# Kernel tuning notes

Measured on AMD Instinct MI355X. Metric: run time of the kernel, lower is better.

The kernel has to match this reference:

```python
import jax, jax.numpy as jnp
import numpy as np

T = 16          # timesteps
BATCH = 8       # video clips -> leading dim of x is BATCH*T = 128
C_IN = 768      # fixed by nn.Conv2d(768, redu_dim, 1)
D = 256         # redu_dim
K = 64          # num_centers
H = W = 28
EPS = 1e-12     # torch F.normalize eps


def _conv(x, w, padding):
    # x: [N,C,H,W], w: [O,I,kh,kw]
    return jax.lax.conv_general_dilated(
        x, w, window_strides=(1, 1), padding=padding,
        dimension_numbers=('NCHW', 'OIHW', 'NCHW'))


def setup_inputs() -> dict:
    key = jax.random.key(0)
    ks = jax.random.split(key, 9)
    x = jax.random.normal(ks[0], (BATCH * T, C_IN, H, W), dtype=jnp.float32)
    redu_w = jax.random.normal(ks[1], (D, C_IN, 1, 1), jnp.float32) * 0.02
    redu_b = jnp.zeros((D,), jnp.float32)
    share_w = jax.random.normal(ks[2], (K, D, 1, 1), jnp.float32) * 0.05
    share_b = jnp.zeros((K,), jnp.float32)
    U_z = jax.random.normal(ks[3], (K, K, 3, 3), jnp.float32) * 0.04
    U_r = jax.random.normal(ks[4], (K, K, 3, 3), jnp.float32) * 0.04
    U_h = jax.random.normal(ks[5], (K, K, 3, 3), jnp.float32) * 0.04
    centers = jax.random.normal(ks[6], (K, D), jnp.float32) * 0.06
    return {"x": x, "redu_w": redu_w, "redu_b": redu_b,
            "share_w": share_w, "share_b": share_b,
            "U_z": U_z, "U_r": U_r, "U_h": U_h,
            "centers": centers, "timesteps": T}


def reference(x, redu_w, redu_b, share_w, share_b, U_z, U_r, U_h, centers, timesteps):
    t = timesteps
    bt, _, h, w = x.shape
    b = bt // t
    k = share_w.shape[0]
    d = redu_w.shape[0]

    # channel reduction (1x1 conv)
    xr = _conv(x, redu_w, 'VALID') + redu_b[None, :, None, None]        # [bt,d,h,w]
    # shared assignment logits (1x1 conv)
    wxb = _conv(xr, share_w, 'VALID') + share_b[None, :, None, None]     # [bt,k,h,w]
    wxb = wxb.reshape(b, t, k, h, w).transpose(1, 0, 2, 3, 4)            # [t,b,k,h,w]

    # sequential ConvGRU over timesteps
    h0 = jnp.zeros((b, k, h, w), x.dtype)
    def step(h_tm1, w_t):
        z = jax.nn.sigmoid(w_t + _conv(h_tm1, U_z, 'SAME'))
        r = jax.nn.sigmoid(w_t + _conv(h_tm1, U_r, 'SAME'))
        hh = jnp.tanh(w_t + _conv(r * h_tm1, U_h, 'SAME'))
        h_new = (1.0 - z) * hh + z * h_tm1
        return h_new, h_new
    _, hs = jax.lax.scan(step, h0, wxb)                                  # [t,b,k,h,w]

    assign = hs.transpose(1, 0, 2, 3, 4).reshape(b * t, k, h * w)        # [bt,k,hw]
    # softmax over centers per spatial location
    assign = jax.nn.softmax(assign, axis=1)

    # VLAD aggregation
    a_sum = assign.sum(axis=-1, keepdims=True)                           # [bt,k,1]
    a = a_sum * centers[None]                                            # [bt,k,d]
    xf = xr.reshape(b * t, d, h * w)                                     # [bt,d,hw]
    vlad = jnp.einsum('bkp,bdp->bkd', assign, xf) - a                    # [bt,k,d]

    vlad = vlad.reshape(b, t, k, d).sum(axis=1)                          # [b,k,d]
    # intra-norm over feature dim, then global L2 norm
    vlad = vlad / jnp.maximum(jnp.linalg.norm(vlad, axis=2, keepdims=True), EPS)
    vlad = vlad.reshape(b, k * d)
    vlad = vlad / jnp.maximum(jnp.linalg.norm(vlad, axis=1, keepdims=True), EPS)
    return vlad
```

## Files before the change

### kernel.cpp

```cpp
#include <hip/hip_runtime.h>
#include <hip/hip_bf16.h>

#define T_ 16
#define B_ 8
#define CIN 768
#define D_ 256
#define K_ 64
#define HW 784
#define W_ 28

typedef short short8 __attribute__((ext_vector_type(8)));
typedef short short4v __attribute__((ext_vector_type(4)));
typedef float floatx4 __attribute__((ext_vector_type(4)));
typedef unsigned short ushort_t;

__device__ __forceinline__ unsigned short f2bf(float x) {
    union { float f; unsigned u; } v; v.f = x;
    unsigned u = v.u;
    unsigned r = (u + 0x7fffu + ((u >> 16) & 1u)) >> 16;
    return (unsigned short)r;
}
__device__ __forceinline__ float bf2f(unsigned short h) {
    union { unsigned u; float f; } v; v.u = ((unsigned)h) << 16; return v.f;
}

__device__ __forceinline__ float block_reduce_sum_256(float v) {
    for (int off = 32; off > 0; off >>= 1) v += __shfl_down(v, off, 64);
    __shared__ float red[4];
    __shared__ float tot;
    int lane = threadIdx.x & 63, wid = threadIdx.x >> 6;
    if (lane == 0) red[wid] = v;
    __syncthreads();
    if (threadIdx.x == 0) tot = red[0] + red[1] + red[2] + red[3];
    __syncthreads();
    return tot;
}

__global__ __launch_bounds__(256) void cvt_weights(
    const float* __restrict__ rw, const float* __restrict__ sw,
    const float* __restrict__ Uz, const float* __restrict__ Ur,
    const float* __restrict__ Uh,
    ushort_t* __restrict__ whi, ushort_t* __restrict__ wlo,
    ushort_t* __restrict__ shi, ushort_t* __restrict__ slo,
    ushort_t* __restrict__ azh, ushort_t* __restrict__ azl,
    ushort_t* __restrict__ ahh, ushort_t* __restrict__ ahl)
{
    int i = blockIdx.x * 256 + threadIdx.x;
    const int nR = D_ * CIN;
    const int nS = K_ * D_;
    const int nZR = 128 * 576;
    const int nH = 64 * 576;
    if (i < nR) {
        float x = rw[i];
        unsigned short h = f2bf(x);
        whi[i] = h; wlo[i] = f2bf(x - bf2f(h));
    } else if (i < nR + nS) {
        int j = i - nR;
        float x = sw[j];
        unsigned short h = f2bf(x);
        shi[j] = h; slo[j] = f2bf(x - bf2f(h));
    } else if (i < nR + nS + nZR) {
        int j = i - nR - nS;
        int row = j / 576, kk = j - row * 576;
        int tap = kk >> 6, c = kk & 63;
        const float* U = (row < 64) ? Uz : Ur;
        float x = U[(((size_t)(row & 63)) * 64 + c) * 9 + tap];
        unsigned short h = f2bf(x);
        azh[j] = h; azl[j] = f2bf(x - bf2f(h));
    } else if (i < nR + nS + nZR + nH) {
        int j = i - nR - nS - nZR;
        int row = j / 576, kk = j - row * 576;
        int tap = kk >> 6, c = kk & 63;
        float x = Uh[(((size_t)row) * 64 + c) * 9 + tap];
        unsigned short h = f2bf(x);
        ahh[j] = h; ahl[j] = f2bf(x - bf2f(h));
    }
}

template<int BM, int KD>
__global__ __launch_bounds__(256, 2) void mfma_conv1x1(
    const float* __restrict__ X, const ushort_t* __restrict__ Whi,
    const ushort_t* __restrict__ Wlo, const float* __restrict__ bias,
    float* __restrict__ Out)
{
    const int nt = blockIdx.x, bt = blockIdx.z;
    const int p0 = nt * 112;
    const int tid = threadIdx.x, lane = tid & 63, wv = tid >> 6;
    const float* Xb = X + (size_t)bt * KD * HW;
    float* Ob = Out + (size_t)bt * BM * HW;

    __shared__ ushort_t lB[2][112 * 40];

    constexpr int NI = (BM == 256) ? 7 : 2;
    constexpr int NKS = KD / 32;
    floatx4 acc[4][NI];
#pragma unroll
    for (int a = 0; a < 4; ++a)
#pragma unroll
        for (int b = 0; b < NI; ++b) acc[a][b] = (floatx4){0.f, 0.f, 0.f, 0.f};

    const int koff = (lane >> 4) * 8;
    const int li = lane & 15;
    const int mbase = (BM == 256) ? wv * 64 : 0;

    const int u0j = tid / 112, u0p = tid - u0j * 112;
    const bool u1v = tid < 192;
    const int u1j = (tid + 256) / 112, u1p = (tid + 256) - u1j * 112;

    float b0[16], b1[16];
    short8 ahi[4], alo[4];

    auto loadB = [&](int k0, float* bb) {
        const float* xp0 = Xb + (size_t)(k0 + u0j * 8) * HW + p0 + u0p;
#pragma unroll
        for (int c = 0; c < 8; ++c) bb[c] = xp0[c * HW];
        if (u1v) {
            const float* xp1 = Xb + (size_t)(k0 + u1j * 8) * HW + p0 + u1p;
#pragma unroll
            for (int c = 0; c < 8; ++c) bb[8 + c] = xp1[c * HW];
        }
    };
    auto writeB = [&](const float* bb) {
        short8 vh, vl;
#pragma unroll
        for (int c = 0; c < 8; ++c) {
            unsigned short h = f2bf(bb[c]);
            vh[c] = (short)h; vl[c] = (short)f2bf(bb[c] - bf2f(h));
        }
        *(short8*)&lB[0][u0p * 40 + u0j * 8] = vh;
        *(short8*)&lB[1][u0p * 40 + u0j * 8] = vl;
        if (u1v) {
#pragma unroll
            for (int c = 0; c < 8; ++c) {
                unsigned short h = f2bf(bb[8 + c]);
                vh[c] = (short)h; vl[c] = (short)f2bf(bb[8 + c] - bf2f(h));
            }
            *(short8*)&lB[0][u1p * 40 + u1j * 8] = vh;
            *(short8*)&lB[1][u1p * 40 + u1j * 8] = vl;
        }
    };
    auto loadA = [&](int k0) {
#pragma unroll
        for (int mi = 0; mi < 4; ++mi) {
            int m = mbase + mi * 16 + li;
            ahi[mi] = *(const short8*)(Whi + (size_t)m * KD + k0 + koff);
            alo[mi] = *(const short8*)(Wlo + (size_t)m * KD + k0 + koff);
        }
    };
    auto domfma = [&]() {
        if constexpr (BM == 256) {
#pragma unroll
            for (int ni = 0; ni < 7; ++ni) {
                int n = ni * 16 + li;
                short8 bhi = *(const short8*)&lB[0][n * 40 + koff];
                short8 blo = *(const short8*)&lB[1][n * 40 + koff];
#pragma unroll
                for (int mi = 0; mi < 4; ++mi) {
                    acc[mi][ni] = __builtin_amdgcn_mfma_f32_16x16x32_bf16(ahi[mi], bhi, acc[mi][ni], 0, 0, 0);
                    acc[mi][ni] = __builtin_amdgcn_mfma_f32_16x16x32_bf16(ahi[mi], blo, acc[mi][ni], 0, 0, 0);
                    acc[mi][ni] = __builtin_amdgcn_mfma_f32_16x16x32_bf16(alo[mi], bhi, acc[mi][ni], 0, 0, 0);
                }
            }
        } else {
#pragma unroll
            for (int nj = 0; nj < 2; ++nj) {
                int ni = wv * 2 + nj;
                if (ni >= 7) break;
                int n = ni * 16 + li;
                short8 bhi = *(const short8*)&lB[0][n * 40 + koff];
                short8 blo = *(const short8*)&lB[1][n * 40 + koff];
#pragma unroll
                for (int mi = 0; mi < 4; ++mi) {
                    acc[mi][nj] = __builtin_amdgcn_mfma_f32_16x16x32_bf16(ahi[mi], bhi, acc[mi][nj], 0, 0, 0);
                    acc[mi][nj] = __builtin_amdgcn_mfma_f32_16x16x32_bf16(ahi[mi], blo, acc[mi][nj], 0, 0, 0);
                    acc[mi][nj] = __builtin_amdgcn_mfma_f32_16x16x32_bf16(alo[mi], bhi, acc[mi][nj], 0, 0, 0);
                }
            }
        }
    };

    loadB(0, b0);
    for (int ks = 0; ks < NKS; ks += 2) {
        loadA(ks * 32);
        writeB(b0);
        __syncthreads();
        if (ks + 1 < NKS) loadB((ks + 1) * 32, b1);
        domfma();
        __syncthreads();
        loadA((ks + 1) * 32);
        writeB(b1);
        __syncthreads();
        if (ks + 2 < NKS) loadB((ks + 2) * 32, b0);
        domfma();
        __syncthreads();
    }

    if constexpr (BM == 256) {
#pragma unroll
        for (int mi = 0; mi < 4; ++mi) {
            int m0g = wv * 64 + mi * 16 + ((lane >> 4) << 2);
#pragma unroll
            for (int ni = 0; ni < 7; ++ni) {
                int p = p0 + ni * 16 + li;
#pragma unroll
                for (int r = 0; r < 4; ++r)
                    Ob[(size_t)(m0g + r) * HW + p] = acc[mi][ni][r] + bias[m0g + r];
            }
        }
    } else {
#pragma unroll
        for (int nj = 0; nj < 2; ++nj) {
            int ni = wv * 2 + nj;
            if (ni >= 7) break;
            int p = p0 + ni * 16 + li;
#pragma unroll
            for (int mi = 0; mi < 4; ++mi) {
                int m0g = mi * 16 + ((lane >> 4) << 2);
#pragma unroll
                for (int r = 0; r < 4; ++r)
                    Ob[(size_t)(m0g + r) * HW + p] = acc[mi][nj][r] + bias[m0g + r];
            }
        }
    }
}

__global__ __launch_bounds__(512, 2) void gru_step(
    const ushort_t* __restrict__ hRhi, const ushort_t* __restrict__ hRlo,
    ushort_t* __restrict__ hWhi, ushort_t* __restrict__ hWlo,
    const ushort_t* __restrict__ azh, const ushort_t* __restrict__ azl,
    const ushort_t* __restrict__ ahh, const ushort_t* __restrict__ ahl,
    const float* __restrict__ wxb, float* __restrict__ hs_t, int t)
{
    const int y0 = blockIdx.x, b = blockIdx.y;
    const int tid = threadIdx.x, lane = tid & 63, wv = tid >> 6;
    const int li = lane & 15, koff8 = (lane >> 4) * 8, kq = (lane >> 4) * 4;

    __shared__ ushort_t Hhi[5 * 30 * 72], Hlo[5 * 30 * 72];
    __shared__ ushort_t Rhi[3 * 30 * 72], Rlo[3 * 30 * 72];
    __shared__ float zs[28 * 68];

    {
        const ushort_t* gh = hRhi + (size_t)b * HW * 64;
        const ushort_t* gl = hRlo + (size_t)b * HW * 64;
        for (int e = tid; e < 1200; e += 512) {
            int r = e / 240, rem = e - r * 240;
            int lx = rem >> 3, j = rem & 7;
            int gy = y0 - 2 + r, gx = lx - 1;
            short8 vh = {0,0,0,0,0,0,0,0}, vl = {0,0,0,0,0,0,0,0};
            if (gy >= 0 && gy < 28 && gx >= 0 && gx < 28) {
                size_t go = ((size_t)(gy * 28 + gx)) * 64 + j * 8;
                vh = *(const short8*)(gh + go);
                vl = *(const short8*)(gl + go);
            }
            int lo = (r * 30 + lx) * 72 + j * 8;
            *(short8*)&Hhi[lo] = vh;
            *(short8*)&Hlo[lo] = vl;
        }
        short8 z8 = {0,0,0,0,0,0,0,0};
        for (int e = tid; e < 1620; e += 512) {
            if (e < 810) *(short8*)&Rhi[e * 8] = z8;
            else         *(short8*)&Rlo[(e - 810) * 8] = z8;
        }
    }
    __syncthreads();

    const float* wx = wxb + ((size_t)(b * T_ + t) * K_) * HW;
    const int c0 = li;
    const int c1 = (li < 12) ? 16 + li : 0;

    if (wv < 4) {
        const int kb = wv * 16;
        const ushort_t* Ah = azh + (size_t)(kb + li) * 576;
        const ushort_t* Al = azl + (size_t)(kb + li) * 576;
        floatx4 az[2];
        az[0] = (floatx4){0.f,0.f,0.f,0.f}; az[1] = (floatx4){0.f,0.f,0.f,0.f};
#pragma unroll
        for (int tap = 0; tap < 9; ++tap) {
            const int dy = tap / 3, dx = tap - dy * 3;
#pragma unroll
            for (int ch = 0; ch < 2; ++ch) {
                short8 whi_ = *(const short8*)(Ah + tap * 64 + ch * 32 + koff8);
                short8 wlo_ = *(const short8*)(Al + tap * 64 + ch * 32 + koff8);
                int cb = ch * 32 + koff8;
                int o0 = ((dy + 1) * 30 + c0 + dx) * 72 + cb;
                int o1 = ((dy + 1) * 30 + c1 + dx) * 72 + cb;
                short8 bh0 = *(const short8*)&Hhi[o0];
                short8 bl0 = *(const short8*)&Hlo[o0];
                short8 bh1 = *(const short8*)&Hhi[o1];
                short8 bl1 = *(const short8*)&Hlo[o1];
                az[0] = __builtin_amdgcn_mfma_f32_16x16x32_bf16(whi_, bh0, az[0], 0, 0, 0);
                az[0] = __builtin_amdgcn_mfma_f32_16x16x32_bf16(whi_, bl0, az[0], 0, 0, 0);
                az[0] = __builtin_amdgcn_mfma_f32_16x16x32_bf16(wlo_, bh0, az[0], 0, 0, 0);
                az[1] = __builtin_amdgcn_mfma_f32_16x16x32_bf16(whi_, bh1, az[1], 0, 0, 0);
                az[1] = __builtin_amdgcn_mfma_f32_16x16x32_bf16(whi_, bl1, az[1], 0, 0, 0);
                az[1] = __builtin_amdgcn_mfma_f32_16x16x32_bf16(wlo_, bh1, az[1], 0, 0, 0);
            }
        }
        const int kb4 = kb + kq;
#pragma unroll
        for (int cf = 0; cf < 2; ++cf) {
            int c = cf * 16 + li;
            if (c < 28) {
                floatx4 zv;
#pragma unroll
                for (int r = 0; r < 4; ++r)
                    zv[r] = 1.f / (1.f + __expf(-(wx[(size_t)(kb4 + r) * HW + y0 * 28 + c] + az[cf][r])));
                *(floatx4*)&zs[c * 68 + kb4] = zv;
            }
        }
    } else {
        const int kb = (wv - 4) * 16;
        const ushort_t* Ah = azh + (size_t)(64 + kb + li) * 576;
        const ushort_t* Al = azl + (size_t)(64 + kb + li) * 576;
        floatx4 ar[3][2];
#pragma unroll
        for (int i = 0; i < 3; ++i) {
            ar[i][0] = (floatx4){0.f,0.f,0.f,0.f};
            ar[i][1] = (floatx4){0.f,0.f,0.f,0.f};
        }
#pragma unroll
        for (int tap = 0; tap < 9; ++tap) {
            const int dy = tap / 3, dx = tap - dy * 3;
#pragma unroll
            for (int ch = 0; ch < 2; ++ch) {
                short8 whi_ = *(const short8*)(Ah + tap * 64 + ch * 32 + koff8);
                short8 wlo_ = *(const short8*)(Al + tap * 64 + ch * 32 + koff8);
                int cb = ch * 32 + koff8;
#pragma unroll
                for (int rr = 0; rr < 3; ++rr) {
                    int o0 = ((rr + dy) * 30 + c0 + dx) * 72 + cb;
                    int o1 = ((rr + dy) * 30 + c1 + dx) * 72 + cb;
                    short8 bh0 = *(const short8*)&Hhi[o0];
                    short8 bl0 = *(const short8*)&Hlo[o0];
                    short8 bh1 = *(const short8*)&Hhi[o1];
                    short8 bl1 = *(const short8*)&Hlo[o1];
                    ar[rr][0] = __builtin_amdgcn_mfma_f32_16x16x32_bf16(whi_, bh0, ar[rr][0], 0, 0, 0);
                    ar[rr][0] = __builtin_amdgcn_mfma_f32_16x16x32_bf16(whi_, bl0, ar[rr][0], 0, 0, 0);
                    ar[rr][0] = __builtin_amdgcn_mfma_f32_16x16x32_bf16(wlo_, bh0, ar[rr][0], 0, 0, 0);
                    ar[rr][1] = __builtin_amdgcn_mfma_f32_16x16x32_bf16(whi_, bh1, ar[rr][1], 0, 0, 0);
                    ar[rr][1] = __builtin_amdgcn_mfma_f32_16x16x32_bf16(whi_, bl1, ar[rr][1], 0, 0, 0);
                    ar[rr][1] = __builtin_amdgcn_mfma_f32_16x16x32_bf16(wlo_, bh1, ar[rr][1], 0, 0, 0);
                }
            }
        }
        const int kb4 = kb + kq;
#pragma unroll
        for (int rr = 0; rr < 3; ++rr) {
            int gy = y0 - 1 + rr;
            if (gy < 0 || gy >= 28) continue;
#pragma unroll
            for (int cf = 0; cf < 2; ++cf) {
                int c = cf * 16 + li;
                if (c >= 28) continue;
                short4v ph = *(const short4v*)&Hhi[((rr + 1) * 30 + c + 1) * 72 + kb4];
                short4v pl = *(const short4v*)&Hlo[((rr + 1) * 30 + c + 1) * 72 + kb4];
                short4v vh, vl;
#pragma unroll
                for (int r = 0; r < 4; ++r) {
                    float rv = 1.f / (1.f + __expf(-(wx[(size_t)(kb4 + r) * HW + gy * 28 + c] + ar[rr][cf][r])));
                    float hv = bf2f((unsigned short)ph[r]) + bf2f((unsigned short)pl[r]);
                    float rh = rv * hv;
                    unsigned short h = f2bf(rh);
                    vh[r] = (short)h; vl[r] = (short)f2bf(rh - bf2f(h));
                }
                *(short4v*)&Rhi[(rr * 30 + c + 1) * 72 + kb4] = vh;
                *(short4v*)&Rlo[(rr * 30 + c + 1) * 72 + kb4] = vl;
            }
        }
    }
    __syncthreads();

    if (wv < 4) {
        const int kb = wv * 16;
        const ushort_t* Ah = ahh + (size_t)(kb + li) * 576;
        const ushort_t* Al = ahl + (size_t)(kb + li) * 576;
        floatx4 ac[2];
        ac[0] = (floatx4){0.f,0.f,0.f,0.f}; ac[1] = (floatx4){0.f,0.f,0.f,0.f};
#pragma unroll
        for (int tap = 0; tap < 9; ++tap) {
            const int dy = tap / 3, dx = tap - dy * 3;
#pragma unroll
            for (int ch = 0; ch < 2; ++ch) {
                short8 whi_ = *(const short8*)(Ah + tap * 64 + ch * 32 + koff8);
                short8 wlo_ = *(const short8*)(Al + tap * 64 + ch * 32 + koff8);
                int cb = ch * 32 + koff8;
                int o0 = (dy * 30 + c0 + dx) * 72 + cb;
                int o1 = (dy * 30 + c1 + dx) * 72 + cb;
                short8 bh0 = *(const short8*)&Rhi[o0];
                short8 bl0 = *(const short8*)&Rlo[o0];
                short8 bh1 = *(const short8*)&Rhi[o1];
                short8 bl1 = *(const short8*)&Rlo[o1];
                ac[0] = __builtin_amdgcn_mfma_f32_16x16x32_bf16(whi_, bh0, ac[0], 0, 0, 0);
                ac[0] = __builtin_amdgcn_mfma_f32_16x16x32_bf16(whi_, bl0, ac[0], 0, 0, 0);
                ac[0] = __builtin_amdgcn_mfma_f32_16x16x32_bf16(wlo_, bh0, ac[0], 0, 0, 0);
                ac[1] = __builtin_amdgcn_mfma_f32_16x16x32_bf16(whi_, bh1, ac[1], 0, 0, 0);
                ac[1] = __builtin_amdgcn_mfma_f32_16x16x32_bf16(whi_, bl1, ac[1], 0, 0, 0);
                ac[1] = __builtin_amdgcn_mfma_f32_16x16x32_bf16(wlo_, bh1, ac[1], 0, 0, 0);
            }
        }
        const int kb4 = kb + kq;
        float* hsb = hs_t + (size_t)b * K_ * HW;
#pragma unroll
        for (int cf = 0; cf < 2; ++cf) {
            int c = cf * 16 + li;
            if (c >= 28) continue;
            int p = y0 * 28 + c;
            floatx4 zv = *(const floatx4*)&zs[c * 68 + kb4];
            short4v ph = *(const short4v*)&Hhi[(2 * 30 + c + 1) * 72 + kb4];
            short4v pl = *(const short4v*)&Hlo[(2 * 30 + c + 1) * 72 + kb4];
            short4v vh, vl;
#pragma unroll
            for (int r = 0; r < 4; ++r) {
                int k = kb4 + r;
                float xv = wx[(size_t)k * HW + p] + ac[cf][r];
                float e2 = __expf(2.f * xv);
                float th = 1.f - 2.f / (e2 + 1.f);
                float hp = bf2f((unsigned short)ph[r]) + bf2f((unsigned short)pl[r]);
                float hn = (1.f - zv[r]) * th + zv[r] * hp;
                hsb[(size_t)k * HW + p] = hn;
                unsigned short h = f2bf(hn);
                vh[r] = (short)h; vl[r] = (short)f2bf(hn - bf2f(h));
            }
            size_t o = ((size_t)(b * HW) + p) * 64 + kb4;
            *(short4v*)(hWhi + o) = vh;
            *(short4v*)(hWlo + o) = vl;
        }
    }
}

__global__ __launch_bounds__(256) void softmax_k(float* __restrict__ hs)
{
    int q = blockIdx.x;
    int py = blockIdx.y;
    float* base = hs + (size_t)q * K_ * HW;
    for (int p = py * 392 + threadIdx.x; p < (py + 1) * 392 && p < HW; p += 256) {
        float v[64];
        float m = -1e30f;
#pragma unroll
        for (int k = 0; k < 64; ++k) {
            v[k] = base[(size_t)k * HW + p];
            m = fmaxf(m, v[k]);
        }
        float s = 0.f;
#pragma unroll
        for (int k = 0; k < 64; ++k) {
            v[k] = __expf(v[k] - m);
            s += v[k];
        }
        float inv = 1.f / s;
#pragma unroll
        for (int k = 0; k < 64; ++k)
            base[(size_t)k * HW + p] = v[k] * inv;
    }
}

__global__ __launch_bounds__(256) void asum_k(const float* __restrict__ hs,
                                              float* __restrict__ asum)
{
    int bid = blockIdx.x; int b = bid >> 6, k = bid & 63;
    float s = 0.f;
    for (int t = 0; t < T_; ++t) {
        const float* row = hs + (((size_t)t * B_ + b) * K_ + k) * HW;
        for (int p = threadIdx.x; p < HW; p += 256) s += row[p];
    }
    float tot = block_reduce_sum_256(s);
    if (threadIdx.x == 0) asum[bid] = tot;
}

__global__ __launch_bounds__(256) void vlad_k(const float* __restrict__ assign,
    const float* __restrict__ xr, float* __restrict__ vladt)
{
    int dt = blockIdx.x, t = blockIdx.y, b = blockIdx.z;
    int q = t * B_ + b, bt = b * T_ + t, d0 = dt * 64;
    const float* ab = assign + (size_t)q * K_ * HW;
    const float* xb = xr + (size_t)bt * D_ * HW;
    __shared__ float As[16][68];
    __shared__ float Xs[16][68];
    int tx = threadIdx.x & 15, ty = threadIdx.x >> 4;
    float acc[4][4] = {{0.f}};

    for (int p0 = 0; p0 < HW; p0 += 16) {
#pragma unroll
        for (int it = 0; it < 4; ++it) {
            int e = threadIdx.x + it * 256;
            int row = e >> 4, pp = e & 15;
            As[pp][row] = ab[(size_t)row * HW + p0 + pp];
            Xs[pp][row] = xb[(size_t)(d0 + row) * HW + p0 + pp];
        }
        __syncthreads();
#pragma unroll
        for (int pp = 0; pp < 16; ++pp) {
            float4 a = *(const float4*)&As[pp][ty * 4];
            float4 xv = *(const float4*)&Xs[pp][tx * 4];
            float av[4] = {a.x, a.y, a.z, a.w};
            float xvv[4] = {xv.x, xv.y, xv.z, xv.w};
#pragma unroll
            for (int r = 0; r < 4; ++r)
#pragma unroll
                for (int s = 0; s < 4; ++s)
                    acc[r][s] = fmaf(av[r], xvv[s], acc[r][s]);
        }
        __syncthreads();
    }
#pragma unroll
    for (int r = 0; r < 4; ++r) {
        int k = ty * 4 + r;
        float4 o = {acc[r][0], acc[r][1], acc[r][2], acc[r][3]};
        *(float4*)&vladt[((size_t)bt * K_ + k) * D_ + d0 + tx * 4] = o;
    }
}

__global__ __launch_bounds__(256) void norm1_k(const float* __restrict__ vladt,
    const float* __restrict__ asum, const float* __restrict__ centers,
    float* __restrict__ out)
{
    int bid = blockIdx.x; int b = bid >> 6, k = bid & 63; int d = threadIdx.x;
    float acc = 0.f;
#pragma unroll
    for (int t = 0; t < T_; ++t)
        acc += vladt[(((size_t)b * T_ + t) * K_ + k) * D_ + d];
    acc -= asum[bid] * centers[(size_t)k * D_ + d];
    float ss = block_reduce_sum_256(acc * acc);
    float n = fmaxf(sqrtf(ss), 1e-12f);
    out[((size_t)b * K_ + k) * D_ + d] = acc / n;
}

__global__ __launch_bounds__(256) void norm2_k(float* __restrict__ out)
{
    int b = blockIdx.x;
    float* v = out + (size_t)b * (K_ * D_);
    float s = 0.f;
    for (int i = threadIdx.x; i < K_ * D_; i += 256) {
        float x = v[i];
        s = fmaf(x, x, s);
    }
    float tot = block_reduce_sum_256(s);
    float n = fmaxf(sqrtf(tot), 1e-12f);
    for (int i = threadIdx.x; i < K_ * D_; i += 256) v[i] = v[i] / n;
}

extern "C" void kernel_launch(void* const* d_in, const int* in_sizes, int n_in,
                              void* d_out, int out_size, void* d_ws, size_t ws_size,
                              hipStream_t stream)
{
    const float* x       = (const float*)d_in[0];
    const float* redu_w  = (const float*)d_in[1];
    const float* redu_b  = (const float*)d_in[2];
    const float* share_w = (const float*)d_in[3];
    const float* share_b = (const float*)d_in[4];
    const float* Uz      = (const float*)d_in[5];
    const float* Ur      = (const float*)d_in[6];
    const float* Uh      = (const float*)d_in[7];
    const float* centers = (const float*)d_in[8];

    float* ws = (float*)d_ws;
    const size_t SZ_XR   = (size_t)128 * D_ * HW;
    const size_t SZ_WXB  = (size_t)128 * K_ * HW;
    const size_t SZ_HS   = (size_t)T_ * B_ * K_ * HW;
    const size_t SZ_PLANE= (size_t)B_ * K_ * HW;

    float* xr    = ws;
    float* wxb   = xr + SZ_XR;
    float* hs    = wxb + SZ_WXB;
    float* asumb = hs + SZ_HS;
    float* wsplit= asumb + 512;
    float* area  = wsplit + 323584;

    ushort_t* whi = (ushort_t*)wsplit;
    ushort_t* wlo = whi + 196608;
    ushort_t* shi = wlo + 196608;
    ushort_t* slo = shi + 16384;
    ushort_t* azh = slo + 16384;
    ushort_t* azl = azh + 73728;
    ushort_t* ahh = azl + 73728;
    ushort_t* ahl = ahh + 36864;

    float* vladt = area;
    ushort_t* st = (ushort_t*)area;
    ushort_t* h0hi = st;
    ushort_t* h0lo = st + SZ_PLANE;
    ushort_t* h1hi = st + 2 * SZ_PLANE;
    ushort_t* h1lo = st + 3 * SZ_PLANE;

    hipMemsetAsync(h0hi, 0, 2 * SZ_PLANE * sizeof(ushort_t), stream);

    cvt_weights<<<dim3((D_ * CIN + K_ * D_ + 128 * 576 + 64 * 576 + 255) / 256),
                  256, 0, stream>>>(redu_w, share_w, Uz, Ur, Uh,
                                    whi, wlo, shi, slo, azh, azl, ahh, ahl);

    mfma_conv1x1<256, CIN><<<dim3(7, 1, 128), 256, 0, stream>>>(x, whi, wlo, redu_b, xr);
    mfma_conv1x1<64, D_><<<dim3(7, 1, 128), 256, 0, stream>>>(xr, shi, slo, share_b, wxb);

    for (int t = 0; t < T_; ++t) {
        const ushort_t* rh_ = (t & 1) ? h1hi : h0hi;
        const ushort_t* rl_ = (t & 1) ? h1lo : h0lo;
        ushort_t* wh_ = (t & 1) ? h0hi : h1hi;
        ushort_t* wl_ = (t & 1) ? h0lo : h1lo;
        gru_step<<<dim3(28, 8), 512, 0, stream>>>(rh_, rl_, wh_, wl_,
                                                  azh, azl, ahh, ahl,
                                                  wxb, hs + (size_t)t * SZ_PLANE, t);
    }

    softmax_k<<<dim3(128, 2), 256, 0, stream>>>(hs);
    asum_k<<<512, 256, 0, stream>>>(hs, asumb);

    vlad_k<<<dim3(4, 16, 8), 256, 0, stream>>>(hs, xr, vladt);
    norm1_k<<<512, 256, 0, stream>>>(vladt, asumb, centers, (float*)d_out);
    norm2_k<<<8, 256, 0, stream>>>((float*)d_out);
}
```

Measured before the change: 674.2 us.

## Make GRU a persistent kernel with grid barrier and fuse assignment sums into VLAD

Replaces the sixteen per-timestep GRU launches with one persistent kernel of 224 blocks that loops over timesteps and synchronises through an atomic-counter grid barrier. This is meant to remove per-step launch overhead and tail gaps. It also drops the separate asum kernel: per-(bt,k) assignment sums are accumulated inside vlad_k and reduced over time in norm1_k. The barrier relies on all 224 blocks being co-resident; if they are not, the kernel deadlocks.

```diff
diff --git a/kernel.cpp b/kernel.cpp
--- a/kernel.cpp
+++ b/kernel.cpp
@@ -8,6 +8,7 @@
 #define K_ 64
 #define HW 784
 #define W_ 28
+#define NBLK 224u
 
 typedef short short8 __attribute__((ext_vector_type(8)));
 typedef short short4v __attribute__((ext_vector_type(4)));
@@ -34,6 +35,18 @@
     if (threadIdx.x == 0) tot = red[0] + red[1] + red[2] + red[3];
     __syncthreads();
     return tot;
+}
+
+__device__ __forceinline__ void grid_sync(unsigned* cnt, unsigned target) {
+    __threadfence();
+    __syncthreads();
+    if (threadIdx.x == 0) {
+        atomicAdd(cnt, 1u);
+        while (__hip_atomic_load(cnt, __ATOMIC_RELAXED, __HIP_MEMORY_SCOPE_AGENT) < target)
+            __builtin_amdgcn_s_sleep(2);
+    }
+    __syncthreads();
+    __threadfence();
 }
 
 __global__ __launch_bounds__(256) void cvt_weights(
@@ -224,207 +237,219 @@
     }
 }
 
-__global__ __launch_bounds__(512, 2) void gru_step(
-    const ushort_t* __restrict__ hRhi, const ushort_t* __restrict__ hRlo,
-    ushort_t* __restrict__ hWhi, ushort_t* __restrict__ hWlo,
+__global__ __launch_bounds__(512, 2) void gru_persist(
+    ushort_t* __restrict__ h0hi, ushort_t* __restrict__ h0lo,
+    ushort_t* __restrict__ h1hi, ushort_t* __restrict__ h1lo,
     const ushort_t* __restrict__ azh, const ushort_t* __restrict__ azl,
     const ushort_t* __restrict__ ahh, const ushort_t* __restrict__ ahl,
-    const float* __restrict__ wxb, float* __restrict__ hs_t, int t)
+    const float* __restrict__ wxb, float* __restrict__ hs, unsigned* cnt)
 {
     const int y0 = blockIdx.x, b = blockIdx.y;
     const int tid = threadIdx.x, lane = tid & 63, wv = tid >> 6;
     const int li = lane & 15, koff8 = (lane >> 4) * 8, kq = (lane >> 4) * 4;
+    const size_t SZP = (size_t)B_ * K_ * HW;
 
     __shared__ ushort_t Hhi[5 * 30 * 72], Hlo[5 * 30 * 72];
     __shared__ ushort_t Rhi[3 * 30 * 72], Rlo[3 * 30 * 72];
     __shared__ float zs[28 * 68];
 
-    {
-        const ushort_t* gh = hRhi + (size_t)b * HW * 64;
-        const ushort_t* gl = hRlo + (size_t)b * HW * 64;
-        for (int e = tid; e < 1200; e += 512) {
-            int r = e / 240, rem = e - r * 240;
-            int lx = rem >> 3, j = rem & 7;
-            int gy = y0 - 2 + r, gx = lx - 1;
-            short8 vh = {0,0,0,0,0,0,0,0}, vl = {0,0,0,0,0,0,0,0};
-            if (gy >= 0 && gy < 28 && gx >= 0 && gx < 28) {
-                size_t go = ((size_t)(gy * 28 + gx)) * 64 + j * 8;
-                vh = *(const short8*)(gh + go);
-                vl = *(const short8*)(gl + go);
-            }
-            int lo = (r * 30 + lx) * 72 + j * 8;
-            *(short8*)&Hhi[lo] = vh;
-            *(short8*)&Hlo[lo] = vl;
-        }
-        short8 z8 = {0,0,0,0,0,0,0,0};
-        for (int e = tid; e < 1620; e += 512) {
-            if (e < 810) *(short8*)&Rhi[e * 8] = z8;
-            else         *(short8*)&Rlo[(e - 810) * 8] = z8;
-        }
-    }
-    __syncthreads();
-
-    const float* wx = wxb + ((size_t)(b * T_ + t) * K_) * HW;
-    const int c0 = li;
-    const int c1 = (li < 12) ? 16 + li : 0;
-
-    if (wv < 4) {
-        const int kb = wv * 16;
-        const ushort_t* Ah = azh + (size_t)(kb + li) * 576;
-        const ushort_t* Al = azl + (size_t)(kb + li) * 576;
-        floatx4 az[2];
-        az[0] = (floatx4){0.f,0.f,0.f,0.f}; az[1] = (floatx4){0.f,0.f,0.f,0.f};
-#pragma unroll
-        for (int tap = 0; tap < 9; ++tap) {
-            const int dy = tap / 3, dx = tap - dy * 3;
-#pragma unroll
-            for (int ch = 0; ch < 2; ++ch) {
-                short8 whi_ = *(const short8*)(Ah + tap * 64 + ch * 32 + koff8);
-                short8 wlo_ = *(const short8*)(Al + tap * 64 + ch * 32 + koff8);
-                int cb = ch * 32 + koff8;
-                int o0 = ((dy + 1) * 30 + c0 + dx) * 72 + cb;
-                int o1 = ((dy + 1) * 30 + c1 + dx) * 72 + cb;
-                short8 bh0 = *(const short8*)&Hhi[o0];
-                short8 bl0 = *(const short8*)&Hlo[o0];
-                short8 bh1 = *(const short8*)&Hhi[o1];
-                short8 bl1 = *(const short8*)&Hlo[o1];
-                az[0] = __builtin_amdgcn_mfma_f32_16x16x32_bf16(whi_, bh0, az[0], 0, 0, 0);
-                az[0] = __builtin_amdgcn_mfma_f32_16x16x32_bf16(whi_, bl0, az[0], 0, 0, 0);
-                az[0] = __builtin_amdgcn_mfma_f32_16x16x32_bf16(wlo_, bh0, az[0], 0, 0, 0);
-                az[1] = __builtin_amdgcn_mfma_f32_16x16x32_bf16(whi_, bh1, az[1], 0, 0, 0);
-                az[1] = __builtin_amdgcn_mfma_f32_16x16x32_bf16(whi_, bl1, az[1], 0, 0, 0);
-                az[1] = __builtin_amdgcn_mfma_f32_16x16x32_bf16(wlo_, bh1, az[1], 0, 0, 0);
-            }
-        }
-        const int kb4 = kb + kq;
-#pragma unroll
-        for (int cf = 0; cf < 2; ++cf) {
-            int c = cf * 16 + li;
-            if (c < 28) {
-                floatx4 zv;
-#pragma unroll
-                for (int r = 0; r < 4; ++r)
-                    zv[r] = 1.f / (1.f + __expf(-(wx[(size_t)(kb4 + r) * HW + y0 * 28 + c] + az[cf][r])));
-                *(floatx4*)&zs[c * 68 + kb4] = zv;
-            }
-        }
-    } else {
-        const int kb = (wv - 4) * 16;
-        const ushort_t* Ah = azh + (size_t)(64 + kb + li) * 576;
-        const ushort_t* Al = azl + (size_t)(64 + kb + li) * 576;
-        floatx4 ar[3][2];
-#pragma unroll
-        for (int i = 0; i < 3; ++i) {
-            ar[i][0] = (floatx4){0.f,0.f,0.f,0.f};
-            ar[i][1] = (floatx4){0.f,0.f,0.f,0.f};
-        }
-#pragma unroll
-        for (int tap = 0; tap < 9; ++tap) {
-            const int dy = tap / 3, dx = tap - dy * 3;
-#pragma unroll
-            for (int ch = 0; ch < 2; ++ch) {
-                short8 whi_ = *(const short8*)(Ah + tap * 64 + ch * 32 + koff8);
-                short8 wlo_ = *(const short8*)(Al + tap * 64 + ch * 32 + koff8);
-                int cb = ch * 32 + koff8;
-#pragma unroll
-                for (int rr = 0; rr < 3; ++rr) {
-                    int o0 = ((rr + dy) * 30 + c0 + dx) * 72 + cb;
-                    int o1 = ((rr + dy) * 30 + c1 + dx) * 72 + cb;
+#pragma unroll 1
+    for (int t = 0; t < T_; ++t) {
+        const ushort_t* hRhi = (t & 1) ? h1hi : h0hi;
+        const ushort_t* hRlo = (t & 1) ? h1lo : h0lo;
+        ushort_t* hWhi = (t & 1) ? h0hi : h1hi;
+        ushort_t* hWlo = (t & 1) ? h0lo : h1lo;
+        float* hs_t = hs + (size_t)t * SZP;
+
+        {
+            const ushort_t* gh = hRhi + (size_t)b * HW * 64;
+            const ushort_t* gl = hRlo + (size_t)b * HW * 64;
+            for (int e = tid; e < 1200; e += 512) {
+                int r = e / 240, rem = e - r * 240;
+                int lx = rem >> 3, j = rem & 7;
+                int gy = y0 - 2 + r, gx = lx - 1;
+                short8 vh = {0,0,0,0,0,0,0,0}, vl = {0,0,0,0,0,0,0,0};
+                if (gy >= 0 && gy < 28 && gx >= 0 && gx < 28) {
+                    size_t go = ((size_t)(gy * 28 + gx)) * 64 + j * 8;
+                    vh = *(const short8*)(gh + go);
+                    vl = *(const short8*)(gl + go);
+                }
+                int lo = (r * 30 + lx) * 72 + j * 8;
+                *(short8*)&Hhi[lo] = vh;
+                *(short8*)&Hlo[lo] = vl;
+            }
+            short8 z8 = {0,0,0,0,0,0,0,0};
+            for (int e = tid; e < 1620; e += 512) {
+                if (e < 810) *(short8*)&Rhi[e * 8] = z8;
+                else         *(short8*)&Rlo[(e - 810) * 8] = z8;
+            }
+        }
+        __syncthreads();
+
+        const float* wx = wxb + ((size_t)(b * T_ + t) * K_) * HW;
+        const int c0 = li;
+        const int c1 = (li < 12) ? 16 + li : 0;
+
+        if (wv < 4) {
+            const int kb = wv * 16;
+            const ushort_t* Ah = azh + (size_t)(kb + li) * 576;
+            const ushort_t* Al = azl + (size_t)(kb + li) * 576;
+            floatx4 az[2];
+            az[0] = (floatx4){0.f,0.f,0.f,0.f}; az[1] = (floatx4){0.f,0.f,0.f,0.f};
+#pragma unroll
+            for (int tap = 0; tap < 9; ++tap) {
+                const int dy = tap / 3, dx = tap - dy * 3;
+#pragma unroll
+                for (int ch = 0; ch < 2; ++ch) {
+                    short8 whi_ = *(const short8*)(Ah + tap * 64 + ch * 32 + koff8);
+                    short8 wlo_ = *(const short8*)(Al + tap * 64 + ch * 32 + koff8);
+                    int cb = ch * 32 + koff8;
+                    int o0 = ((dy + 1) * 30 + c0 + dx) * 72 + cb;
+                    int o1 = ((dy + 1) * 30 + c1 + dx) * 72 + cb;
                     short8 bh0 = *(const short8*)&Hhi[o0];
                     short8 bl0 = *(const short8*)&Hlo[o0];
                     short8 bh1 = *(const short8*)&Hhi[o1];
                     short8 bl1 = *(const short8*)&Hlo[o1];
-                    ar[rr][0] = __builtin_amdgcn_mfma_f32_16x16x32_bf16(whi_, bh0, ar[rr][0], 0, 0, 0);
-                    ar[rr][0] = __builtin_amdgcn_mfma_f32_16x16x32_bf16(whi_, bl0, ar[rr][0], 0, 0, 0);
-                    ar[rr][0] = __builtin_amdgcn_mfma_f32_16x16x32_bf16(wlo_, bh0, ar[rr][0], 0, 0, 0);
-                    ar[rr][1] = __builtin_amdgcn_mfma_f32_16x16x32_bf16(whi_, bh1, ar[rr][1], 0, 0, 0);
-                    ar[rr][1] = __builtin_amdgcn_mfma_f32_16x16x32_bf16(whi_, bl1, ar[rr][1], 0, 0, 0);
-                    ar[rr][1] = __builtin_amdgcn_mfma_f32_16x16x32_bf16(wlo_, bh1, ar[rr][1], 0, 0, 0);
-                }
-            }
-        }
-        const int kb4 = kb + kq;
-#pragma unroll
-        for (int rr = 0; rr < 3; ++rr) {
-            int gy = y0 - 1 + rr;
-            if (gy < 0 || gy >= 28) continue;
+                    az[0] = __builtin_amdgcn_mfma_f32_16x16x32_bf16(whi_, bh0, az[0], 0, 0, 0);
+                    az[0] = __builtin_amdgcn_mfma_f32_16x16x32_bf16(whi_, bl0, az[0], 0, 0, 0);
+                    az[0] = __builtin_amdgcn_mfma_f32_16x16x32_bf16(wlo_, bh0, az[0], 0, 0, 0);
+                    az[1] = __builtin_amdgcn_mfma_f32_16x16x32_bf16(whi_, bh1, az[1], 0, 0, 0);
+                    az[1] = __builtin_amdgcn_mfma_f32_16x16x32_bf16(whi_, bl1, az[1], 0, 0, 0);
+                    az[1] = __builtin_amdgcn_mfma_f32_16x16x32_bf16(wlo_, bh1, az[1], 0, 0, 0);
+                }
+            }
+            const int kb4 = kb + kq;
+#pragma unroll
+            for (int cf = 0; cf < 2; ++cf) {
+                int c = cf * 16 + li;
+                if (c < 28) {
+                    floatx4 zv;
+#pragma unroll
+                    for (int r = 0; r < 4; ++r)
+                        zv[r] = 1.f / (1.f + __expf(-(wx[(size_t)(kb4 + r) * HW + y0 * 28 + c] + az[cf][r])));
+                    *(floatx4*)&zs[c * 68 + kb4] = zv;
+                }
+            }
+        } else {
+            const int kb = (wv - 4) * 16;
+            const ushort_t* Ah = azh + (size_t)(64 + kb + li) * 576;
+            const ushort_t* Al = azl + (size_t)(64 + kb + li) * 576;
+            floatx4 ar[3][2];
+#pragma unroll
+            for (int i = 0; i < 3; ++i) {
+                ar[i][0] = (floatx4){0.f,0.f,0.f,0.f};
+                ar[i][1] = (floatx4){0.f,0.f,0.f,0.f};
+            }
+#pragma unroll
+            for (int tap = 0; tap < 9; ++tap) {
+                const int dy = tap / 3, dx = tap - dy * 3;
+#pragma unroll
+                for (int ch = 0; ch < 2; ++ch) {
+                    short8 whi_ = *(const short8*)(Ah + tap * 64 + ch * 32 + koff8);
+                    short8 wlo_ = *(const short8*)(Al + tap * 64 + ch * 32 + koff8);
+                    int cb = ch * 32 + koff8;
+#pragma unroll
+                    for (int rr = 0; rr < 3; ++rr) {
+                        int o0 = ((rr + dy) * 30 + c0 + dx) * 72 + cb;
+                        int o1 = ((rr + dy) * 30 + c1 + dx) * 72 + cb;
+                        short8 bh0 = *(const short8*)&Hhi[o0];
+                        short8 bl0 = *(const short8*)&Hlo[o0];
+                        short8 bh1 = *(const short8*)&Hhi[o1];
+                        short8 bl1 = *(const short8*)&Hlo[o1];
+                        ar[rr][0] = __builtin_amdgcn_mfma_f32_16x16x32_bf16(whi_, bh0, ar[rr][0], 0, 0, 0);
+                        ar[rr][0] = __builtin_amdgcn_mfma_f32_16x16x32_bf16(whi_, bl0, ar[rr][0], 0, 0, 0);
+                        ar[rr][0] = __builtin_amdgcn_mfma_f32_16x16x32_bf16(wlo_, bh0, ar[rr][0], 0, 0, 0);
+                        ar[rr][1] = __builtin_amdgcn_mfma_f32_16x16x32_bf16(whi_, bh1, ar[rr][1], 0, 0, 0);
+                        ar[rr][1] = __builtin_amdgcn_mfma_f32_16x16x32_bf16(whi_, bl1, ar[rr][1], 0, 0, 0);
+                        ar[rr][1] = __builtin_amdgcn_mfma_f32_16x16x32_bf16(wlo_, bh1, ar[rr][1], 0, 0, 0);
+                    }
+                }
+            }
+            const int kb4 = kb + kq;
+#pragma unroll
+            for (int rr = 0; rr < 3; ++rr) {
+                int gy = y0 - 1 + rr;
+                if (gy < 0 || gy >= 28) continue;
+#pragma unroll
+                for (int cf = 0; cf < 2; ++cf) {
+                    int c = cf * 16 + li;
+                    if (c >= 28) continue;
+                    short4v ph = *(const short4v*)&Hhi[((rr + 1) * 30 + c + 1) * 72 + kb4];
+                    short4v pl = *(const short4v*)&Hlo[((rr + 1) * 30 + c + 1) * 72 + kb4];
+                    short4v vh, vl;
+#pragma unroll
+                    for (int r = 0; r < 4; ++r) {
+                        float rv = 1.f / (1.f + __expf(-(wx[(size_t)(kb4 + r) * HW + gy * 28 + c] + ar[rr][cf][r])));
+                        float hv = bf2f((unsigned short)ph[r]) + bf2f((unsigned short)pl[r]);
+                        float rh = rv * hv;
+                        unsigned short h = f2bf(rh);
+                        vh[r] = (short)h; vl[r] = (short)f2bf(rh - bf2f(h));
+                    }
+                    *(short4v*)&Rhi[(rr * 30 + c + 1) * 72 + kb4] = vh;
+                    *(short4v*)&Rlo[(rr * 30 + c + 1) * 72 + kb4] = vl;
+                }
+            }
+        }
+        __syncthreads();
+
+        if (wv < 4) {
+            const int kb = wv * 16;
+            const ushort_t* Ah = ahh + (size_t)(kb + li) * 576;
+            const ushort_t* Al = ahl + (size_t)(kb + li) * 576;
+            floatx4 ac[2];
+            ac[0] = (floatx4){0.f,0.f,0.f,0.f}; ac[1] = (floatx4){0.f,0.f,0.f,0.f};
+#pragma unroll
+            for (int tap = 0; tap < 9; ++tap) {
+                const int dy = tap / 3, dx = tap - dy * 3;
+#pragma unroll
+                for (int ch = 0; ch < 2; ++ch) {
+                    short8 whi_ = *(const short8*)(Ah + tap * 64 + ch * 32 + koff8);
+                    short8 wlo_ = *(const short8*)(Al + tap * 64 + ch * 32 + koff8);
+                    int cb = ch * 32 + koff8;
+                    int o0 = (dy * 30 + c0 + dx) * 72 + cb;
+                    int o1 = (dy * 30 + c1 + dx) * 72 + cb;
+                    short8 bh0 = *(const short8*)&Rhi[o0];
+                    short8 bl0 = *(const short8*)&Rlo[o0];
+                    short8 bh1 = *(const short8*)&Rhi[o1];
+                    short8 bl1 = *(const short8*)&Rlo[o1];
+                    ac[0] = __builtin_amdgcn_mfma_f32_16x16x32_bf16(whi_, bh0, ac[0], 0, 0, 0);
+                    ac[0] = __builtin_amdgcn_mfma_f32_16x16x32_bf16(whi_, bl0, ac[0], 0, 0, 0);
+                    ac[0] = __builtin_amdgcn_mfma_f32_16x16x32_bf16(wlo_, bh0, ac[0], 0, 0, 0);
+                    ac[1] = __builtin_amdgcn_mfma_f32_16x16x32_bf16(whi_, bh1, ac[1], 0, 0, 0);
+                    ac[1] = __builtin_amdgcn_mfma_f32_16x16x32_bf16(whi_, bl1, ac[1], 0, 0, 0);
+                    ac[1] = __builtin_amdgcn_mfma_f32_16x16x32_bf16(wlo_, bh1, ac[1], 0, 0, 0);
+                }
+            }
+            const int kb4 = kb + kq;
+            float* hsb = hs_t + (size_t)b * K_ * HW;
 #pragma unroll
             for (int cf = 0; cf < 2; ++cf) {
                 int c = cf * 16 + li;
                 if (c >= 28) continue;
-                short4v ph = *(const short4v*)&Hhi[((rr + 1) * 30 + c + 1) * 72 + kb4];
-                short4v pl = *(const short4v*)&Hlo[((rr + 1) * 30 + c + 1) * 72 + kb4];
+                int p = y0 * 28 + c;
+                floatx4 zv = *(const floatx4*)&zs[c * 68 + kb4];
+                short4v ph = *(const short4v*)&Hhi[(2 * 30 + c + 1) * 72 + kb4];
+                short4v pl = *(const short4v*)&Hlo[(2 * 30 + c + 1) * 72 + kb4];
                 short4v vh, vl;
 #pragma unroll
                 for (int r = 0; r < 4; ++r) {
-                    float rv = 1.f / (1.f + __expf(-(wx[(size_t)(kb4 + r) * HW + gy * 28 + c] + ar[rr][cf][r])));
-                    float hv = bf2f((unsigned short)ph[r]) + bf2f((unsigned short)pl[r]);
-                    float rh = rv * hv;
-                    unsigned short h = f2bf(rh);
-                    vh[r] = (short)h; vl[r] = (short)f2bf(rh - bf2f(h));
-                }
-                *(short4v*)&Rhi[(rr * 30 + c + 1) * 72 + kb4] = vh;
-                *(short4v*)&Rlo[(rr * 30 + c + 1) * 72 + kb4] = vl;
-            }
-        }
-    }
-    __syncthreads();
-
-    if (wv < 4) {
-        const int kb = wv * 16;
-        const ushort_t* Ah = ahh + (size_t)(kb + li) * 576;
-        const ushort_t* Al = ahl + (size_t)(kb + li) * 576;
-        floatx4 ac[2];
-        ac[0] = (floatx4){0.f,0.f,0.f,0.f}; ac[1] = (floatx4){0.f,0.f,0.f,0.f};
-#pragma unroll
-        for (int tap = 0; tap < 9; ++tap) {
-            const int dy = tap / 3, dx = tap - dy * 3;
-#pragma unroll
-            for (int ch = 0; ch < 2; ++ch) {
-                short8 whi_ = *(const short8*)(Ah + tap * 64 + ch * 32 + koff8);
-                short8 wlo_ = *(const short8*)(Al + tap * 64 + ch * 32 + koff8);
-                int cb = ch * 32 + koff8;
-                int o0 = (dy * 30 + c0 + dx) * 72 + cb;
-                int o1 = (dy * 30 + c1 + dx) * 72 + cb;
-                short8 bh0 = *(const short8*)&Rhi[o0];
-                short8 bl0 = *(const short8*)&Rlo[o0];
-                short8 bh1 = *(const short8*)&Rhi[o1];
-                short8 bl1 = *(const short8*)&Rlo[o1];
-                ac[0] = __builtin_amdgcn_mfma_f32_16x16x32_bf16(whi_, bh0, ac[0], 0, 0, 0);
-                ac[0] = __builtin_amdgcn_mfma_f32_16x16x32_bf16(whi_, bl0, ac[0], 0, 0, 0);
-                ac[0] = __builtin_amdgcn_mfma_f32_16x16x32_bf16(wlo_, bh0, ac[0], 0, 0, 0);
-                ac[1] = __builtin_amdgcn_mfma_f32_16x16x32_bf16(whi_, bh1, ac[1], 0, 0, 0);
-                ac[1] = __builtin_amdgcn_mfma_f32_16x16x32_bf16(whi_, bl1, ac[1], 0, 0, 0);
-                ac[1] = __builtin_amdgcn_mfma_f32_16x16x32_bf16(wlo_, bh1, ac[1], 0, 0, 0);
-            }
-        }
-        const int kb4 = kb + kq;
-        float* hsb = hs_t + (size_t)b * K_ * HW;
-#pragma unroll
-        for (int cf = 0; cf < 2; ++cf) {
-            int c = cf * 16 + li;
-            if (c >= 28) continue;
-            int p = y0 * 28 + c;
-            floatx4 zv = *(const floatx4*)&zs[c * 68 + kb4];
-            short4v ph = *(const short4v*)&Hhi[(2 * 30 + c + 1) * 72 + kb4];
-            short4v pl = *(const short4v*)&Hlo[(2 * 30 + c + 1) * 72 + kb4];
-            short4v vh, vl;
-#pragma unroll
-            for (int r = 0; r < 4; ++r) {
-                int k = kb4 + r;
-                float xv = wx[(size_t)k * HW + p] + ac[cf][r];
-                float e2 = __expf(2.f * xv);
-                float th = 1.f - 2.f / (e2 + 1.f);
-                float hp = bf2f((unsigned short)ph[r]) + bf2f((unsigned short)pl[r]);
-                float hn = (1.f - zv[r]) * th + zv[r] * hp;
-                hsb[(size_t)k * HW + p] = hn;
-                unsigned short h = f2bf(hn);
-                vh[r] = (short)h; vl[r] = (short)f2bf(hn - bf2f(h));
-            }
-            size_t o = ((size_t)(b * HW) + p) * 64 + kb4;
-            *(short4v*)(hWhi + o) = vh;
-            *(short4v*)(hWlo + o) = vl;
-        }
+                    int k = kb4 + r;
+                    float xv = wx[(size_t)k * HW + p] + ac[cf][r];
+                    float e2 = __expf(2.f * xv);
+                    float th = 1.f - 2.f / (e2 + 1.f);
+                    float hp = bf2f((unsigned short)ph[r]) + bf2f((unsigned short)pl[r]);
+                    float hn = (1.f - zv[r]) * th + zv[r] * hp;
+                    hsb[(size_t)k * HW + p] = hn;
+                    unsigned short h = f2bf(hn);
+                    vh[r] = (short)h; vl[r] = (short)f2bf(hn - bf2f(h));
+                }
+                size_t o = ((size_t)(b * HW) + p) * 64 + kb4;
+                *(short4v*)(hWhi + o) = vh;
+                *(short4v*)(hWlo + o) = vl;
+            }
+        }
+
+        if (t + 1 < T_) grid_sync(cnt, NBLK * (unsigned)(t + 1));
     }
 }
 
@@ -454,21 +479,9 @@
     }
 }
 
-__global__ __launch_bounds__(256) void asum_k(const float* __restrict__ hs,
-                                              float* __restrict__ asum)
-{
-    int bid = blockIdx.x; int b = bid >> 6, k = bid & 63;
-    float s = 0.f;
-    for (int t = 0; t < T_; ++t) {
-        const float* row = hs + (((size_t)t * B_ + b) * K_ + k) * HW;
-        for (int p = threadIdx.x; p < HW; p += 256) s += row[p];
-    }
-    float tot = block_reduce_sum_256(s);
-    if (threadIdx.x == 0) asum[bid] = tot;
-}
-
 __global__ __launch_bounds__(256) void vlad_k(const float* __restrict__ assign,
-    const float* __restrict__ xr, float* __restrict__ vladt)
+    const float* __restrict__ xr, float* __restrict__ vladt,
+    float* __restrict__ asum_bt)
 {
     int dt = blockIdx.x, t = blockIdx.y, b = blockIdx.z;
     int q = t * B_ + b, bt = b * T_ + t, d0 = dt * 64;
@@ -478,13 +491,16 @@
     __shared__ float Xs[16][68];
     int tx = threadIdx.x & 15, ty = threadIdx.x >> 4;
     float acc[4][4] = {{0.f}};
+    float pacc[4] = {0.f, 0.f, 0.f, 0.f};
 
     for (int p0 = 0; p0 < HW; p0 += 16) {
 #pragma unroll
         for (int it = 0; it < 4; ++it) {
             int e = threadIdx.x + it * 256;
             int row = e >> 4, pp = e & 15;
-            As[pp][row] = ab[(size_t)row * HW + p0 + pp];
+            float av_ = ab[(size_t)row * HW + p0 + pp];
+            As[pp][row] = av_;
+            if (dt == 0) pacc[it] += av_;
             Xs[pp][row] = xb[(size_t)(d0 + row) * HW + p0 + pp];
         }
         __syncthreads();
@@ -508,10 +524,19 @@
         float4 o = {acc[r][0], acc[r][1], acc[r][2], acc[r][3]};
         *(float4*)&vladt[((size_t)bt * K_ + k) * D_ + d0 + tx * 4] = o;
     }
+    if (dt == 0) {
+#pragma unroll
+        for (int it = 0; it < 4; ++it) {
+            float s = pacc[it];
+#pragma unroll
+            for (int off = 1; off < 16; off <<= 1) s += __shfl_xor(s, off, 16);
+            if (tx == 0) asum_bt[(size_t)bt * 64 + ty + it * 16] = s;
+        }
+    }
 }
 
 __global__ __launch_bounds__(256) void norm1_k(const float* __restrict__ vladt,
-    const float* __restrict__ asum, const float* __restrict__ centers,
+    const float* __restrict__ asum_bt, const float* __restrict__ centers,
     float* __restrict__ out)
 {
     int bid = blockIdx.x; int b = bid >> 6, k = bid & 63; int d = threadIdx.x;
@@ -519,7 +544,11 @@
 #pragma unroll
     for (int t = 0; t < T_; ++t)
         acc += vladt[(((size_t)b * T_ + t) * K_ + k) * D_ + d];
-    acc -= asum[bid] * centers[(size_t)k * D_ + d];
+    float asum = 0.f;
+#pragma unroll
+    for (int t = 0; t < T_; ++t)
+        asum += asum_bt[(size_t)(b * T_ + t) * 64 + k];
+    acc -= asum * centers[(size_t)k * D_ + d];
     float ss = block_reduce_sum_256(acc * acc);
     float n = fmaxf(sqrtf(ss), 1e-12f);
     out[((size_t)b * K_ + k) * D_ + d] = acc / n;
@@ -559,12 +588,13 @@
     const size_t SZ_HS   = (size_t)T_ * B_ * K_ * HW;
     const size_t SZ_PLANE= (size_t)B_ * K_ * HW;
 
-    float* xr    = ws;
-    float* wxb   = xr + SZ_XR;
-    float* hs    = wxb + SZ_WXB;
-    float* asumb = hs + SZ_HS;
-    float* wsplit= asumb + 512;
-    float* area  = wsplit + 323584;
+    float* xr     = ws;
+    float* wxb    = xr + SZ_XR;
+    float* hs     = wxb + SZ_WXB;
+    float* asum_bt= hs + SZ_HS;
+    unsigned* cnt = (unsigned*)(asum_bt + 8192);
+    float* wsplit = asum_bt + 8192 + 64;
+    float* area   = wsplit + 323584;
 
     ushort_t* whi = (ushort_t*)wsplit;
     ushort_t* wlo = whi + 196608;
@@ -583,6 +613,7 @@
     ushort_t* h1lo = st + 3 * SZ_PLANE;
 
     hipMemsetAsync(h0hi, 0, 2 * SZ_PLANE * sizeof(ushort_t), stream);
+    hipMemsetAsync(cnt, 0, 256, stream);
 
     cvt_weights<<<dim3((D_ * CIN + K_ * D_ + 128 * 576 + 64 * 576 + 255) / 256),
                   256, 0, stream>>>(redu_w, share_w, Uz, Ur, Uh,
@@ -591,20 +622,12 @@
     mfma_conv1x1<256, CIN><<<dim3(7, 1, 128), 256, 0, stream>>>(x, whi, wlo, redu_b, xr);
     mfma_conv1x1<64, D_><<<dim3(7, 1, 128), 256, 0, stream>>>(xr, shi, slo, share_b, wxb);
 
-    for (int t = 0; t < T_; ++t) {
-        const ushort_t* rh_ = (t & 1) ? h1hi : h0hi;
-        const ushort_t* rl_ = (t & 1) ? h1lo : h0lo;
-        ushort_t* wh_ = (t & 1) ? h0hi : h1hi;
-        ushort_t* wl_ = (t & 1) ? h0lo : h1lo;
-        gru_step<<<dim3(28, 8), 512, 0, stream>>>(rh_, rl_, wh_, wl_,
-                                                  azh, azl, ahh, ahl,
-                                                  wxb, hs + (size_t)t * SZ_PLANE, t);
-    }
+    gru_persist<<<dim3(28, 8), 512, 0, stream>>>(h0hi, h0lo, h1hi, h1lo,
+                                                 azh, azl, ahh, ahl, wxb, hs, cnt);
 
     softmax_k<<<dim3(128, 2), 256, 0, stream>>>(hs);
-    asum_k<<<512, 256, 0, stream>>>(hs, asumb);
-
-    vlad_k<<<dim3(4, 16, 8), 256, 0, stream>>>(hs, xr, vladt);
-    norm1_k<<<512, 256, 0, stream>>>(vladt, asumb, centers, (float*)d_out);
+
+    vlad_k<<<dim3(4, 16, 8), 256, 0, stream>>>(hs, xr, vladt, asum_bt);
+    norm1_k<<<512, 256, 0, stream>>>(vladt, asum_bt, centers, (float*)d_out);
     norm2_k<<<8, 256, 0, stream>>>((float*)d_out);
 }
```

Measured after the change: 1.914 ms. 2.84x slower.
